# Kernel optimization log

Measured on AMD Instinct MI355X. Metric: run time of the kernel, lower is better.

The kernel has to match this reference:

```python
import jax, jax.numpy as jnp
import numpy as np

NUM_CLASSES = 64
CDF_DIM = 128
EMBED_DIM = 1024
BATCH = 16


def setup_inputs() -> dict:
    key = jax.random.key(0)
    k_x, k_w1, k_b1, k_w2, k_b2 = jax.random.split(key, 5)
    bound1 = 1.0 / np.sqrt(EMBED_DIM)
    x = jax.random.normal(k_x, (BATCH, NUM_CLASSES * CDF_DIM, EMBED_DIM), dtype=jnp.float32)
    # stacked per-class weights: W1 [C,E,E] (applied as x @ W1), b1 [C,E], W2 [C,E], b2 [C]
    W1 = jax.random.uniform(k_w1, (NUM_CLASSES, EMBED_DIM, EMBED_DIM), jnp.float32, -bound1, bound1)
    b1 = jax.random.uniform(k_b1, (NUM_CLASSES, EMBED_DIM), jnp.float32, -bound1, bound1)
    W2 = jax.random.uniform(k_w2, (NUM_CLASSES, EMBED_DIM), jnp.float32, -bound1, bound1)
    b2 = jax.random.uniform(k_b2, (NUM_CLASSES,), jnp.float32, -bound1, bound1)
    return {"x": x, "W1": W1, "b1": b1, "W2": W2, "b2": b2}


def reference(x, W1, b1, W2, b2):
    B = x.shape[0]
    # [B, C, T, E] where T = cdf_dim
    xr = x.reshape(B, NUM_CLASSES, CDF_DIM, EMBED_DIM)
    # per-class first Linear + exact GELU (torch default is erf-based)
    h = jnp.einsum('bcte,ceo->bcto', xr, W1) + b1[None, :, None, :]
    h = jax.nn.gelu(h, approximate=False)
    # per-class second Linear to scalar, squeeze
    out = jnp.einsum('bcte,ce->bct', h, W2) + b2[None, :, None]
    # concat over classes -> [B, C*T]
    return out.reshape(B, NUM_CLASSES * CDF_DIM)
```

## Files before the change

### kernel.cpp

```cpp
#include <hip/hip_runtime.h>
#include <hip/hip_bf16.h>
#include <math.h>

#define NCLS 64
#define TDIM 128
#define EMB  1024
#define NBATCH 16

#define BM 128
#define BN 128
#define BK 32
#define NT (EMB / BK)
#define BUFSH 8192

typedef __attribute__((ext_vector_type(8))) short bfrag8;
typedef __attribute__((ext_vector_type(4))) float ffrag4;

__device__ __forceinline__ unsigned int pk2(float lo, float hi) {
    union { __hip_bfloat162 h; unsigned int u; } cv;
    cv.h = __float22bfloat162_rn(make_float2(lo, hi));
    return cv.u;
}
__device__ __forceinline__ short f2bs(float f) {
    return (short)(pk2(f, 0.f) & 0xffff);
}

union S8 { bfrag8 s; unsigned int u[4]; };

__device__ __forceinline__ void async16(const short* g, const short* l) {
    __builtin_amdgcn_global_load_lds(
        (const __attribute__((address_space(1))) unsigned int*)(unsigned long long)(uintptr_t)g,
        (__attribute__((address_space(3))) unsigned int*)(unsigned int)(uintptr_t)l,
        16, 0, 0);
}

__device__ __forceinline__ float gelu_fast(float h) {
    float az = fabsf(h) * 0.70710678118654752f;
    float t  = __builtin_amdgcn_rcpf(fmaf(0.3275911f, az, 1.0f));
    float p  = fmaf(1.061405429f, t, -1.453152027f);
    p = fmaf(p, t, 1.421413741f);
    p = fmaf(p, t, -0.284496736f);
    p = fmaf(p, t, 0.254829592f);
    p = p * t;
    float e = __expf(-az * az);
    float y = fmaf(-p, e, 1.0f);
    return fmaf(0.5f * fabsf(h), y, 0.5f * h);
}

__global__ __launch_bounds__(256) void init_out(const float* __restrict__ b2,
                                                float* __restrict__ out) {
    int i = blockIdx.x * 256 + threadIdx.x;
    int c = (i >> 7) & (NCLS - 1);
    out[i] = b2[c];
}

__global__ __launch_bounds__(256) void cvt_x(const float* __restrict__ x,
                                             short* __restrict__ xb) {
    size_t i = ((size_t)blockIdx.x * 256 + threadIdx.x) * 8;
    float4 a = *(const float4*)(x + i);
    float4 b = *(const float4*)(x + i + 4);
    S8 p;
    p.u[0] = pk2(a.x, a.y); p.u[1] = pk2(a.z, a.w);
    p.u[2] = pk2(b.x, b.y); p.u[3] = pk2(b.z, b.w);
    *(bfrag8*)(xb + i) = p.s;
}

__global__ __launch_bounds__(256) void cvt_w1t(const float* __restrict__ W1,
                                               short* __restrict__ w1t) {
    const int bid = blockIdx.x;
    const int nt = bid & 15, kt = (bid >> 4) & 15, c = bid >> 8;
    const int t = threadIdx.x;
    __shared__ short ldsT[64 * 72];

    const float* src = W1 + (size_t)c * 1048576 + (size_t)(kt * 64) * 1024 + nt * 64;
    const int kr = t >> 4, nq = (t & 15) * 4;
#pragma unroll
    for (int i = 0; i < 4; ++i) {
        int k = kr + i * 16;
        float4 v = *(const float4*)(src + (size_t)k * 1024 + nq);
        ldsT[(nq + 0) * 72 + k] = f2bs(v.x);
        ldsT[(nq + 1) * 72 + k] = f2bs(v.y);
        ldsT[(nq + 2) * 72 + k] = f2bs(v.z);
        ldsT[(nq + 3) * 72 + k] = f2bs(v.w);
    }
    __syncthreads();
    short* dst = w1t + (size_t)c * 1048576 + (size_t)(nt * 64) * 1024 + kt * 64;
#pragma unroll
    for (int p = 0; p < 2; ++p) {
        int chunk = t + p * 256;
        int n = chunk >> 3, kc = chunk & 7;
        bfrag8 v = *(const bfrag8*)(ldsT + n * 72 + kc * 8);
        *(bfrag8*)(dst + (size_t)n * 1024 + kc * 8) = v;
    }
}

__global__ __launch_bounds__(256, 3) void mlp_gemm(
    const short* __restrict__ xb, const short* __restrict__ w1t,
    const float* __restrict__ b1, const float* __restrict__ W2,
    float* __restrict__ out)
{
    const int bid = blockIdx.x;
    const int xcd = bid & 7;
    const int idx = bid >> 3;
    const int c   = ((idx >> 7) << 3) | xcd;
    const int w   = idx & 127;
    const int mb  = w >> 3;
    const int nb  = w & 7;

    __shared__ __align__(16) short lds[3 * BUFSH];

    const int tid  = threadIdx.x;
    const int lane = tid & 63;
    const int wave = tid >> 6;
    const int wm = wave >> 1, wn = wave & 1;
    const int quad = lane >> 4, l16 = lane & 15;

    const short* gA0 = xb + ((size_t)mb * 8192 + c * 128 + (2 * wave) * 16 + l16) * 1024
                          + quad * 8;
    const short* gA1 = gA0 + 16 * 1024;
    const short* gB0 = w1t + (size_t)c * 1048576
                           + (size_t)(nb * 128 + (2 * wave) * 16 + l16) * 1024 + quad * 8;
    const short* gB1 = gB0 + 16 * 1024;
    const int stA = (2 * wave) * 512;
    const int stB = 4096 + (2 * wave) * 512;

    const int ardo = (wm * 4) * 512 + quad * 128 + l16 * 8;
    const int brdo = 4096 + (wn * 4) * 512 + quad * 128 + l16 * 8;

    ffrag4 acc[4][4] = {};

    async16(gA0, lds + stA);        async16(gA1, lds + stA + 512);
    async16(gB0, lds + stB);        async16(gB1, lds + stB + 512);
    gA0 += BK; gA1 += BK; gB0 += BK; gB1 += BK;
    async16(gA0, lds + BUFSH + stA); async16(gA1, lds + BUFSH + stA + 512);
    async16(gB0, lds + BUFSH + stB); async16(gB1, lds + BUFSH + stB + 512);
    gA0 += BK; gA1 += BK; gB0 += BK; gB1 += BK;
    asm volatile("s_waitcnt vmcnt(4)" ::: "memory");
    __builtin_amdgcn_sched_barrier(0);
    __builtin_amdgcn_s_barrier();
    __builtin_amdgcn_sched_barrier(0);

    int qr = 0;
    int qs = 2;
    for (int t = 0; t < NT; ++t) {
        if (t < NT - 2) {
            const short* sb = lds + qs * BUFSH;
            async16(gA0, sb + stA); async16(gA1, sb + stA + 512);
            async16(gB0, sb + stB); async16(gB1, sb + stB + 512);
            gA0 += BK; gA1 += BK; gB0 += BK; gB1 += BK;
        }
        const short* rb = lds + qr * BUFSH;
        bfrag8 af[4], bf[4];
#pragma unroll
        for (int mi = 0; mi < 4; ++mi) af[mi] = *(const bfrag8*)(rb + ardo + mi * 512);
#pragma unroll
        for (int ni = 0; ni < 4; ++ni) bf[ni] = *(const bfrag8*)(rb + brdo + ni * 512);
        asm volatile("s_waitcnt lgkmcnt(0)" ::: "memory");
        __builtin_amdgcn_sched_barrier(0);
        __builtin_amdgcn_s_setprio(1);
#pragma unroll
        for (int mi = 0; mi < 4; ++mi)
#pragma unroll
            for (int ni = 0; ni < 4; ++ni)
                acc[mi][ni] = __builtin_amdgcn_mfma_f32_16x16x32_bf16(
                    af[mi], bf[ni], acc[mi][ni], 0, 0, 0);
        __builtin_amdgcn_s_setprio(0);
        __builtin_amdgcn_sched_barrier(0);
        if (t < NT - 2) {
            asm volatile("s_waitcnt vmcnt(4)" ::: "memory");
        } else if (t == NT - 2) {
            asm volatile("s_waitcnt vmcnt(0)" ::: "memory");
        }
        if (t < NT - 1) {
            __builtin_amdgcn_sched_barrier(0);
            __builtin_amdgcn_s_barrier();
            __builtin_amdgcn_sched_barrier(0);
        }
        qr = (qr == 2) ? 0 : qr + 1;
        qs = (qs == 2) ? 0 : qs + 1;
    }

    const int nbase = c * 1024 + nb * 128 + wn * 64 + l16;
    float b1v[4], w2v[4];
#pragma unroll
    for (int ni = 0; ni < 4; ++ni) {
        b1v[ni] = b1[nbase + ni * 16];
        w2v[ni] = W2[nbase + ni * 16];
    }

    float* outp = out + (size_t)mb * 8192 + c * 128 + wm * 64 + quad * 4;
#pragma unroll
    for (int mi = 0; mi < 4; ++mi) {
        float s[4] = {0.f, 0.f, 0.f, 0.f};
#pragma unroll
        for (int ni = 0; ni < 4; ++ni) {
#pragma unroll
            for (int r = 0; r < 4; ++r) {
                float h = acc[mi][ni][r] + b1v[ni];
                s[r] += gelu_fast(h) * w2v[ni];
            }
        }
#pragma unroll
        for (int r = 0; r < 4; ++r) {
            s[r] += __shfl_xor(s[r], 8, 64);
            s[r] += __shfl_xor(s[r], 4, 64);
            s[r] += __shfl_xor(s[r], 2, 64);
            s[r] += __shfl_xor(s[r], 1, 64);
            if (l16 == 0) atomicAdd(outp + mi * 16 + r, s[r]);
        }
    }
}

__global__ __launch_bounds__(256) void mlp_head_fallback(
    const float* __restrict__ x,  const float* __restrict__ W1,
    const float* __restrict__ b1, const float* __restrict__ W2,
    float* __restrict__ out)
{
    const int bid = blockIdx.x;
    const int nb = bid & 7;
    const int mb = (bid >> 3) & 15;
    const int c  = bid >> 7;

    __shared__ __align__(16) short lds_a[BM * BK];
    __shared__ __align__(16) short lds_b[BN * BK];

    const int tid  = threadIdx.x;
    const int lane = tid & 63;
    const int wave = tid >> 6;
    const int wm = wave >> 1, wn = wave & 1;
    const int quad = lane >> 4, l16 = lane & 15;

    const int arow = tid & 127;
    const int akh  = tid >> 7;
    const float* aptr = x + ((size_t)mb * 8192 + (size_t)c * 128 + arow) * 1024 + akh * 16;
    short* aw0 = lds_a + (arow >> 4) * 512 + (akh * 2) * 128 + (arow & 15) * 8;
    short* aw1 = aw0 + 128;

    const int ncol = tid & 127;
    const int bkh  = tid >> 7;
    const float* bptr = W1 + (size_t)c * 1024 * 1024 + (size_t)(bkh * 16) * 1024
                           + (size_t)nb * 128 + ncol;
    short* bw0 = lds_b + (ncol >> 4) * 512 + (bkh * 2) * 128 + (ncol & 15) * 8;
    short* bw1 = bw0 + 128;

    const short* ard = lds_a + (wm * 4) * 512 + quad * 128 + l16 * 8;
    const short* brd = lds_b + (wn * 4) * 512 + quad * 128 + l16 * 8;

    ffrag4 acc[4][4] = {};

    for (int kt = 0; kt < EMB / BK; ++kt) {
        float4 a0 = *(const float4*)(aptr + 0);
        float4 a1 = *(const float4*)(aptr + 4);
        float4 a2 = *(const float4*)(aptr + 8);
        float4 a3 = *(const float4*)(aptr + 12);
        float bv[16];
#pragma unroll
        for (int j = 0; j < 16; ++j) bv[j] = bptr[(size_t)j * 1024];
        aptr += BK;
        bptr += (size_t)BK * 1024;

        __syncthreads();

        S8 pa0, pa1, pb0, pb1;
        pa0.u[0] = pk2(a0.x, a0.y); pa0.u[1] = pk2(a0.z, a0.w);
        pa0.u[2] = pk2(a1.x, a1.y); pa0.u[3] = pk2(a1.z, a1.w);
        pa1.u[0] = pk2(a2.x, a2.y); pa1.u[1] = pk2(a2.z, a2.w);
        pa1.u[2] = pk2(a3.x, a3.y); pa1.u[3] = pk2(a3.z, a3.w);
#pragma unroll
        for (int j = 0; j < 4; ++j) pb0.u[j] = pk2(bv[2 * j], bv[2 * j + 1]);
#pragma unroll
        for (int j = 0; j < 4; ++j) pb1.u[j] = pk2(bv[8 + 2 * j], bv[9 + 2 * j]);

        *(bfrag8*)aw0 = pa0.s;
        *(bfrag8*)aw1 = pa1.s;
        *(bfrag8*)bw0 = pb0.s;
        *(bfrag8*)bw1 = pb1.s;

        __syncthreads();

        bfrag8 af[4], bf[4];
#pragma unroll
        for (int mi = 0; mi < 4; ++mi) af[mi] = *(const bfrag8*)(ard + mi * 512);
#pragma unroll
        for (int ni = 0; ni < 4; ++ni) bf[ni] = *(const bfrag8*)(brd + ni * 512);
#pragma unroll
        for (int mi = 0; mi < 4; ++mi)
#pragma unroll
            for (int ni = 0; ni < 4; ++ni)
                acc[mi][ni] = __builtin_amdgcn_mfma_f32_16x16x32_bf16(
                    af[mi], bf[ni], acc[mi][ni], 0, 0, 0);
    }

    const int nbase = c * 1024 + nb * 128 + wn * 64 + l16;
    float b1v[4], w2v[4];
#pragma unroll
    for (int ni = 0; ni < 4; ++ni) {
        b1v[ni] = b1[nbase + ni * 16];
        w2v[ni] = W2[nbase + ni * 16];
    }

    float* outp = out + (size_t)mb * 8192 + c * 128 + wm * 64 + quad * 4;
#pragma unroll
    for (int mi = 0; mi < 4; ++mi) {
        float s[4] = {0.f, 0.f, 0.f, 0.f};
#pragma unroll
        for (int ni = 0; ni < 4; ++ni) {
#pragma unroll
            for (int r = 0; r < 4; ++r) {
                float h = acc[mi][ni][r] + b1v[ni];
                s[r] += gelu_fast(h) * w2v[ni];
            }
        }
#pragma unroll
        for (int r = 0; r < 4; ++r) {
            s[r] += __shfl_xor(s[r], 8, 64);
            s[r] += __shfl_xor(s[r], 4, 64);
            s[r] += __shfl_xor(s[r], 2, 64);
            s[r] += __shfl_xor(s[r], 1, 64);
            if (l16 == 0) atomicAdd(outp + mi * 16 + r, s[r]);
        }
    }
}

extern "C" void kernel_launch(void* const* d_in, const int* in_sizes, int n_in,
                              void* d_out, int out_size, void* d_ws, size_t ws_size,
                              hipStream_t stream) {
    const float* x  = (const float*)d_in[0];
    const float* W1 = (const float*)d_in[1];
    const float* b1 = (const float*)d_in[2];
    const float* W2 = (const float*)d_in[3];
    const float* b2 = (const float*)d_in[4];
    float* out = (float*)d_out;

    const size_t xb_bytes  = (size_t)NBATCH * NCLS * TDIM * EMB * 2;
    const size_t w1t_bytes = (size_t)NCLS * EMB * EMB * 2;

    init_out<<<dim3(512), dim3(256), 0, stream>>>(b2, out);

    if (ws_size >= xb_bytes + w1t_bytes) {
        short* xb  = (short*)d_ws;
        short* w1t = (short*)((char*)d_ws + xb_bytes);
        cvt_x<<<dim3(65536), dim3(256), 0, stream>>>(x, xb);
        cvt_w1t<<<dim3(16384), dim3(256), 0, stream>>>(W1, w1t);
        mlp_gemm<<<dim3(NCLS * 16 * 8), dim3(256), 0, stream>>>(xb, w1t, b1, W2, out);
    } else {
        mlp_head_fallback<<<dim3(NCLS * 16 * 8), dim3(256), 0, stream>>>(x, W1, b1, W2, out);
    }
}
```

Measured before the change: 1.396 ms.

## Use 256x256 tiles with 8 waves, BK=64 and interleaved MFMA/load phases

Result: faster. 1.349 ms (-3.4%).

```diff
diff --git a/kernel.cpp b/kernel.cpp
--- a/kernel.cpp
+++ b/kernel.cpp
@@ -10,8 +10,11 @@
 #define BM 128
 #define BN 128
 #define BK 32
-#define NT (EMB / BK)
-#define BUFSH 8192
+
+#define BK2   64
+#define KT2   (EMB / BK2)
+#define ABUF  16384
+#define BUFSZ 32768
 
 typedef __attribute__((ext_vector_type(8))) short bfrag8;
 typedef __attribute__((ext_vector_type(4))) float ffrag4;
@@ -47,6 +50,12 @@
     return fmaf(0.5f * fabsf(h), y, 0.5f * h);
 }
 
+#define SBAR()  do { __builtin_amdgcn_sched_barrier(0); \
+                     __builtin_amdgcn_s_barrier(); \
+                     __builtin_amdgcn_sched_barrier(0); } while (0)
+#define LGKM0() do { asm volatile("s_waitcnt lgkmcnt(0)" ::: "memory"); \
+                     __builtin_amdgcn_sched_barrier(0); } while (0)
+
 __global__ __launch_bounds__(256) void init_out(const float* __restrict__ b2,
                                                 float* __restrict__ out) {
     int i = blockIdx.x * 256 + threadIdx.x;
@@ -56,13 +65,16 @@
 
 __global__ __launch_bounds__(256) void cvt_x(const float* __restrict__ x,
                                              short* __restrict__ xb) {
-    size_t i = ((size_t)blockIdx.x * 256 + threadIdx.x) * 8;
-    float4 a = *(const float4*)(x + i);
-    float4 b = *(const float4*)(x + i + 4);
-    S8 p;
-    p.u[0] = pk2(a.x, a.y); p.u[1] = pk2(a.z, a.w);
-    p.u[2] = pk2(b.x, b.y); p.u[3] = pk2(b.z, b.w);
-    *(bfrag8*)(xb + i) = p.s;
+    size_t i = ((size_t)blockIdx.x * 256 + threadIdx.x) * 32;
+#pragma unroll
+    for (int j = 0; j < 4; ++j) {
+        float4 a = *(const float4*)(x + i + j * 8);
+        float4 b = *(const float4*)(x + i + j * 8 + 4);
+        S8 p;
+        p.u[0] = pk2(a.x, a.y); p.u[1] = pk2(a.z, a.w);
+        p.u[2] = pk2(b.x, b.y); p.u[3] = pk2(b.z, b.w);
+        *(bfrag8*)(xb + i + j * 8) = p.s;
+    }
 }
 
 __global__ __launch_bounds__(256) void cvt_w1t(const float* __restrict__ W1,
@@ -94,7 +106,7 @@
     }
 }
 
-__global__ __launch_bounds__(256, 3) void mlp_gemm(
+__global__ __launch_bounds__(512, 2) void mlp_gemm8(
     const short* __restrict__ xb, const short* __restrict__ w1t,
     const float* __restrict__ b1, const float* __restrict__ W2,
     float* __restrict__ out)
@@ -102,85 +114,144 @@
     const int bid = blockIdx.x;
     const int xcd = bid & 7;
     const int idx = bid >> 3;
-    const int c   = ((idx >> 7) << 3) | xcd;
-    const int w   = idx & 127;
-    const int mb  = w >> 3;
-    const int nb  = w & 7;
-
-    __shared__ __align__(16) short lds[3 * BUFSH];
+    const int c   = ((idx >> 5) << 3) | xcd;
+    const int w5  = idx & 31;
+    const int mb  = w5 >> 2;
+    const int nb2 = w5 & 3;
+
+    __shared__ __align__(16) short lds[2 * BUFSZ];
 
     const int tid  = threadIdx.x;
     const int lane = tid & 63;
     const int wave = tid >> 6;
-    const int wm = wave >> 1, wn = wave & 1;
+    const int wm = wave >> 2, wn = wave & 3;
     const int quad = lane >> 4, l16 = lane & 15;
-
-    const short* gA0 = xb + ((size_t)mb * 8192 + c * 128 + (2 * wave) * 16 + l16) * 1024
+    const int lo8  = lane * 8;
+
+    const short* gA0 = xb + ((size_t)(mb * 2 + 0) * 8192 + c * 128 + wave * 16 + l16) * 1024
                           + quad * 8;
-    const short* gA1 = gA0 + 16 * 1024;
+    const short* gA1 = xb + ((size_t)(mb * 2 + 1) * 8192 + c * 128 + wave * 16 + l16) * 1024
+                          + quad * 8;
     const short* gB0 = w1t + (size_t)c * 1048576
-                           + (size_t)(nb * 128 + (2 * wave) * 16 + l16) * 1024 + quad * 8;
-    const short* gB1 = gB0 + 16 * 1024;
-    const int stA = (2 * wave) * 512;
-    const int stB = 4096 + (2 * wave) * 512;
-
-    const int ardo = (wm * 4) * 512 + quad * 128 + l16 * 8;
-    const int brdo = 4096 + (wn * 4) * 512 + quad * 128 + l16 * 8;
-
-    ffrag4 acc[4][4] = {};
-
-    async16(gA0, lds + stA);        async16(gA1, lds + stA + 512);
-    async16(gB0, lds + stB);        async16(gB1, lds + stB + 512);
-    gA0 += BK; gA1 += BK; gB0 += BK; gB1 += BK;
-    async16(gA0, lds + BUFSH + stA); async16(gA1, lds + BUFSH + stA + 512);
-    async16(gB0, lds + BUFSH + stB); async16(gB1, lds + BUFSH + stB + 512);
-    gA0 += BK; gA1 += BK; gB0 += BK; gB1 += BK;
-    asm volatile("s_waitcnt vmcnt(4)" ::: "memory");
-    __builtin_amdgcn_sched_barrier(0);
-    __builtin_amdgcn_s_barrier();
-    __builtin_amdgcn_sched_barrier(0);
-
-    int qr = 0;
-    int qs = 2;
-    for (int t = 0; t < NT; ++t) {
-        if (t < NT - 2) {
-            const short* sb = lds + qs * BUFSH;
-            async16(gA0, sb + stA); async16(gA1, sb + stA + 512);
-            async16(gB0, sb + stB); async16(gB1, sb + stB + 512);
-            gA0 += BK; gA1 += BK; gB0 += BK; gB1 += BK;
-        }
-        const short* rb = lds + qr * BUFSH;
-        bfrag8 af[4], bf[4];
-#pragma unroll
-        for (int mi = 0; mi < 4; ++mi) af[mi] = *(const bfrag8*)(rb + ardo + mi * 512);
-#pragma unroll
-        for (int ni = 0; ni < 4; ++ni) bf[ni] = *(const bfrag8*)(rb + brdo + ni * 512);
-        asm volatile("s_waitcnt lgkmcnt(0)" ::: "memory");
-        __builtin_amdgcn_sched_barrier(0);
+                           + (size_t)(nb2 * 256 + wave * 16 + l16) * 1024 + quad * 8;
+    const short* gB1 = gB0 + (size_t)128 * 1024;
+    const int dA0 = (wave * 2) * 512;
+    const int dA1 = ((8 + wave) * 2) * 512;
+    const int dB0 = ABUF + (wave * 2) * 512;
+    const int dB1 = ABUF + ((8 + wave) * 2) * 512;
+
+    ffrag4 acc[8][4] = {};
+    bfrag8 af[4][2], bf[4][2];
+
+#pragma unroll
+    for (int b = 0; b < 2; ++b) {
+        short* dst = (short*)lds + b * BUFSZ;
+        async16(gA0,      dst + dA0);       async16(gA0 + 32, dst + dA0 + 512);
+        async16(gA1,      dst + dA1);       async16(gA1 + 32, dst + dA1 + 512);
+        async16(gB0,      dst + dB0);       async16(gB0 + 32, dst + dB0 + 512);
+        async16(gB1,      dst + dB1);       async16(gB1 + 32, dst + dB1 + 512);
+        gA0 += BK2; gA1 += BK2; gB0 += BK2; gB1 += BK2;
+    }
+    asm volatile("s_waitcnt vmcnt(8)" ::: "memory");
+    SBAR();
+
+    for (int t = 0; t < KT2; ++t) {
+        const short* rb = lds + (t & 1) * BUFSZ;
+        short* sb = (short*)rb;
+        const bool st = (t < KT2 - 2);
+
+#pragma unroll
+        for (int mi = 0; mi < 4; ++mi)
+#pragma unroll
+            for (int kh = 0; kh < 2; ++kh)
+                af[mi][kh] = *(const bfrag8*)(rb + ((wm * 8 + mi) * 2 + kh) * 512 + lo8);
+#pragma unroll
+        for (int ni = 0; ni < 2; ++ni)
+#pragma unroll
+            for (int kh = 0; kh < 2; ++kh)
+                bf[ni][kh] = *(const bfrag8*)(rb + ABUF + ((wn * 4 + ni) * 2 + kh) * 512 + lo8);
+        SBAR();
+        LGKM0();
         __builtin_amdgcn_s_setprio(1);
 #pragma unroll
         for (int mi = 0; mi < 4; ++mi)
 #pragma unroll
-            for (int ni = 0; ni < 4; ++ni)
-                acc[mi][ni] = __builtin_amdgcn_mfma_f32_16x16x32_bf16(
-                    af[mi], bf[ni], acc[mi][ni], 0, 0, 0);
+            for (int ni = 0; ni < 2; ++ni)
+#pragma unroll
+                for (int kh = 0; kh < 2; ++kh)
+                    acc[mi][ni] = __builtin_amdgcn_mfma_f32_16x16x32_bf16(
+                        af[mi][kh], bf[ni][kh], acc[mi][ni], 0, 0, 0);
+        __builtin_amdgcn_s_setprio(0);
+        SBAR();
+
+#pragma unroll
+        for (int ni = 2; ni < 4; ++ni)
+#pragma unroll
+            for (int kh = 0; kh < 2; ++kh)
+                bf[ni][kh] = *(const bfrag8*)(rb + ABUF + ((wn * 4 + ni) * 2 + kh) * 512 + lo8);
+        SBAR();
+        LGKM0();
+        __builtin_amdgcn_s_setprio(1);
+#pragma unroll
+        for (int mi = 0; mi < 4; ++mi)
+#pragma unroll
+            for (int ni = 2; ni < 4; ++ni)
+#pragma unroll
+                for (int kh = 0; kh < 2; ++kh)
+                    acc[mi][ni] = __builtin_amdgcn_mfma_f32_16x16x32_bf16(
+                        af[mi][kh], bf[ni][kh], acc[mi][ni], 0, 0, 0);
+        __builtin_amdgcn_s_setprio(0);
+        SBAR();
+
+#pragma unroll
+        for (int mi = 0; mi < 4; ++mi)
+#pragma unroll
+            for (int kh = 0; kh < 2; ++kh)
+                af[mi][kh] = *(const bfrag8*)(rb + ((wm * 8 + 4 + mi) * 2 + kh) * 512 + lo8);
+        if (st) {
+            async16(gB0,      sb + dB0);    async16(gB0 + 32, sb + dB0 + 512);
+            async16(gB1,      sb + dB1);    async16(gB1 + 32, sb + dB1 + 512);
+        }
+        SBAR();
+        LGKM0();
+        __builtin_amdgcn_s_setprio(1);
+#pragma unroll
+        for (int mi = 0; mi < 4; ++mi)
+#pragma unroll
+            for (int ni = 0; ni < 2; ++ni)
+#pragma unroll
+                for (int kh = 0; kh < 2; ++kh)
+                    acc[4 + mi][ni] = __builtin_amdgcn_mfma_f32_16x16x32_bf16(
+                        af[mi][kh], bf[ni][kh], acc[4 + mi][ni], 0, 0, 0);
+        __builtin_amdgcn_s_setprio(0);
+        SBAR();
+
+        if (st) {
+            async16(gA0,      sb + dA0);    async16(gA0 + 32, sb + dA0 + 512);
+            async16(gA1,      sb + dA1);    async16(gA1 + 32, sb + dA1 + 512);
+            gA0 += BK2; gA1 += BK2; gB0 += BK2; gB1 += BK2;
+        }
+        SBAR();
+        __builtin_amdgcn_s_setprio(1);
+#pragma unroll
+        for (int mi = 0; mi < 4; ++mi)
+#pragma unroll
+            for (int ni = 2; ni < 4; ++ni)
+#pragma unroll
+                for (int kh = 0; kh < 2; ++kh)
+                    acc[4 + mi][ni] = __builtin_amdgcn_mfma_f32_16x16x32_bf16(
+                        af[mi][kh], bf[ni][kh], acc[4 + mi][ni], 0, 0, 0);
         __builtin_amdgcn_s_setprio(0);
         __builtin_amdgcn_sched_barrier(0);
-        if (t < NT - 2) {
-            asm volatile("s_waitcnt vmcnt(4)" ::: "memory");
-        } else if (t == NT - 2) {
+        if (st) {
+            asm volatile("s_waitcnt vmcnt(8)" ::: "memory");
+        } else if (t == KT2 - 2) {
             asm volatile("s_waitcnt vmcnt(0)" ::: "memory");
         }
-        if (t < NT - 1) {
-            __builtin_amdgcn_sched_barrier(0);
-            __builtin_amdgcn_s_barrier();
-            __builtin_amdgcn_sched_barrier(0);
-        }
-        qr = (qr == 2) ? 0 : qr + 1;
-        qs = (qs == 2) ? 0 : qs + 1;
-    }
-
-    const int nbase = c * 1024 + nb * 128 + wn * 64 + l16;
+        if (t < KT2 - 1) SBAR();
+    }
+
+    const int nbase = c * 1024 + nb2 * 256 + wn * 64 + l16;
     float b1v[4], w2v[4];
 #pragma unroll
     for (int ni = 0; ni < 4; ++ni) {
@@ -188,9 +259,9 @@
         w2v[ni] = W2[nbase + ni * 16];
     }
 
-    float* outp = out + (size_t)mb * 8192 + c * 128 + wm * 64 + quad * 4;
-#pragma unroll
-    for (int mi = 0; mi < 4; ++mi) {
+    float* outp = out + (size_t)(mb * 2 + wm) * 8192 + c * 128 + quad * 4;
+#pragma unroll
+    for (int mi = 0; mi < 8; ++mi) {
         float s[4] = {0.f, 0.f, 0.f, 0.f};
 #pragma unroll
         for (int ni = 0; ni < 4; ++ni) {
@@ -340,9 +411,9 @@
     if (ws_size >= xb_bytes + w1t_bytes) {
         short* xb  = (short*)d_ws;
         short* w1t = (short*)((char*)d_ws + xb_bytes);
-        cvt_x<<<dim3(65536), dim3(256), 0, stream>>>(x, xb);
+        cvt_x<<<dim3(16384), dim3(256), 0, stream>>>(x, xb);
         cvt_w1t<<<dim3(16384), dim3(256), 0, stream>>>(W1, w1t);
-        mlp_gemm<<<dim3(NCLS * 16 * 8), dim3(256), 0, stream>>>(xb, w1t, b1, W2, out);
+        mlp_gemm8<<<dim3(2048), dim3(512), 0, stream>>>(xb, w1t, b1, W2, out);
     } else {
         mlp_head_fallback<<<dim3(NCLS * 16 * 8), dim3(256), 0, stream>>>(x, W1, b1, W2, out);
     }
```
